# Optimization experiments

Hardware: AMD Instinct MI355X
Metric: run time of the kernel (lower is better)

## Reference

```python
import jax, jax.numpy as jnp
import numpy as np

NUM_HEADS = 12
DIM_HEAD = 64
SCALE = DIM_HEAD ** -0.5
LOG2PI = float(np.log(2.0 * np.pi))


def setup_inputs() -> dict:
    key = jax.random.key(0)
    k1, k2, k3, k4 = jax.random.split(key, 4)
    b, n, e = 2, 2048, 768
    inner = NUM_HEADS * DIM_HEAD
    return {
        "x": jax.random.normal(k1, (b, n, e), dtype=jnp.float32),
        "w_qkv": jax.random.normal(k2, (e, 3 * inner), dtype=jnp.float32) * (e ** -0.5),
        "w_out": jax.random.normal(k3, (inner, e), dtype=jnp.float32) * (inner ** -0.5),
        "b_out": jax.random.normal(k4, (e,), dtype=jnp.float32) * 0.02,
    }


def reference(x, w_qkv, w_out, b_out):
    b, n, _ = x.shape
    h, d = NUM_HEADS, DIM_HEAD
    qkv = x @ w_qkv  # (b, n, 3*h*d)
    q, k, v = jnp.split(qkv, 3, axis=-1)
    # (b, n, h*d) -> (b, h, n, d)
    to_heads = lambda t: t.reshape(b, n, h, d).transpose(0, 2, 1, 3)
    q, k, v = to_heads(q), to_heads(k), to_heads(v)

    dots = jnp.einsum("bhid,bhjd->bhij", q, k) * SCALE  # (b, h, n, n)
    attn = jax.nn.softmax(dots, axis=-1)
    product = jnp.einsum("bhij,bhjd->bhid", attn, v)  # (b, h, n, d)

    # cross-head statistics (torch.var is unbiased -> ddof=1)
    mean = jnp.mean(product, axis=1, keepdims=True)           # (b, 1, n, d)
    variance = jnp.var(product, axis=1, ddof=1, keepdims=True)  # (b, 1, n, d)

    log_probs = -0.5 * (LOG2PI + jnp.log(variance)
                        - 0.5 * (product - mean) ** 2 / variance)
    log_probs = jnp.sum(log_probs, axis=-1) \
        - jnp.sum(jnp.log(jnp.sqrt(variance)), axis=-1)  # (b, h, n)

    # second attn-weighted matmul, weighted by per-(b,h,n) log-likelihood
    out = jnp.einsum("bhij,bhjd->bhid", log_probs[..., None] * attn, v)
    out = out.transpose(0, 2, 1, 3).reshape(b, n, h * d)  # (b, n, h*d)
    return out @ w_out + b_out
```

## Files before the change

### kernel.cpp

```cpp
#include <hip/hip_runtime.h>

#define BB    2
#define NCTX  2048
#define EDIM  768
#define HH    12
#define DH    64
#define NQKV  2304
#define QSZ   (BB*HH*NCTX*DH)
#define GK    768
#define SCALE 0.125f
#define LOG2PI 1.8378770664093453f

typedef __bf16 bf16x8 __attribute__((ext_vector_type(8)));
typedef __bf16 bf16x4 __attribute__((ext_vector_type(4)));
typedef float  f32x4  __attribute__((ext_vector_type(4)));
typedef float  f32x16 __attribute__((ext_vector_type(16)));

#define GLOAD_LDS16(g, l)                                      \
  __builtin_amdgcn_global_load_lds(                            \
      (const __attribute__((address_space(1))) void*)(g),      \
      (__attribute__((address_space(3))) void*)(l), 16, 0, 0)

__device__ __forceinline__
void cvt_T_tile(const float* __restrict__ W, __bf16* __restrict__ WT,
                int R, int C, int c0, int r0, int t) {
  __shared__ float ts[32][33];
  const int rr = t >> 5, cc = t & 31;
  #pragma unroll
  for (int i = 0; i < 4; ++i)
    ts[rr + i*8][cc] = W[(size_t)(r0 + rr + i*8)*C + c0 + cc];
  __syncthreads();
  #pragma unroll
  for (int i = 0; i < 4; ++i)
    WT[(size_t)(c0 + rr + i*8)*R + r0 + cc] = (__bf16)ts[cc][rr + i*8];
}

__global__ __launch_bounds__(256)
void prep_all(const float* __restrict__ x, __bf16* __restrict__ xbf,
              const float* __restrict__ wqkv, const float* __restrict__ wout,
              __bf16* __restrict__ wqkvT, __bf16* __restrict__ woutT) {
  int b = blockIdx.x;
  if (b < 1536) {
    int i = b*256 + threadIdx.x;
    float4 a = *(const float4*)(x + (size_t)i*8);
    float4 c = *(const float4*)(x + (size_t)i*8 + 4);
    bf16x8 o;
    o[0]=(__bf16)a.x; o[1]=(__bf16)a.y; o[2]=(__bf16)a.z; o[3]=(__bf16)a.w;
    o[4]=(__bf16)c.x; o[5]=(__bf16)c.y; o[6]=(__bf16)c.z; o[7]=(__bf16)c.w;
    *(bf16x8*)(xbf + (size_t)i*8) = o;
  } else if (b < 3264) {
    b -= 1536;
    cvt_T_tile(wqkv, wqkvT, GK, NQKV, (b % 72)*32, (b / 72)*32, threadIdx.x);
  } else {
    b -= 3264;
    cvt_T_tile(wout, woutT, GK, EDIM, (b % 24)*32, (b / 24)*32, threadIdx.x);
  }
}

#define GSTAGE(t_, b_) do {                                                  \
    _Pragma("unroll")                                                        \
    for (int i_ = 0; i_ < 2; ++i_) {                                         \
      GLOAD_LDS16(Asrc + (size_t)i_*16*GK + (size_t)(t_)*32,                 \
                  dstA + (b_)*16384 + i_*1024);                              \
      GLOAD_LDS16(Bsrc + (size_t)i_*16*GK + (size_t)(t_)*32,                 \
                  dstB + (b_)*16384 + i_*1024);                              \
    } } while (0)

#define GITER(ki_, c_) do {                                                  \
    if ((ki_) < GK/32 - 1)                                                   \
      asm volatile("s_waitcnt vmcnt(4)" ::: "memory");                       \
    else                                                                     \
      asm volatile("s_waitcnt vmcnt(0)" ::: "memory");                       \
    __builtin_amdgcn_s_barrier();                                            \
    asm volatile("" ::: "memory");                                           \
    if ((ki_) + 2 < GK/32) GSTAGE((ki_) + 2, ((c_) + 2) % 3);                \
    const char* Asc = smem + (c_)*16384;                                     \
    const char* Bsc = Asc + 8192;                                            \
    bf16x8 af[4], bf[4];                                                     \
    _Pragma("unroll")                                                        \
    for (int mf = 0; mf < 4; ++mf) {                                         \
      int m = wr*64 + mf*16 + l15;                                           \
      af[mf] = *(const bf16x8*)(Asc + m*64 + ((g*16) ^ (((m>>1)&3)<<4)));    \
    }                                                                        \
    _Pragma("unroll")                                                        \
    for (int nf = 0; nf < 4; ++nf) {                                         \
      int n = wc*64 + nf*16 + l15;                                           \
      bf[nf] = *(const bf16x8*)(Bsc + n*64 + ((g*16) ^ (((n>>1)&3)<<4)));    \
    }                                                                        \
    __builtin_amdgcn_s_setprio(1);                                           \
    _Pragma("unroll")                                                        \
    for (int mf = 0; mf < 4; ++mf)                                           \
      _Pragma("unroll")                                                      \
      for (int nf = 0; nf < 4; ++nf)                                         \
        acc[mf][nf] = __builtin_amdgcn_mfma_f32_16x16x32_bf16(               \
            af[mf], bf[nf], acc[mf][nf], 0, 0, 0);                           \
    __builtin_amdgcn_s_setprio(0);                                           \
  } while (0)

#define GEMM_CORE(Aa, Bb, acc)                                               \
  const int lane = tid & 63, w = tid >> 6;                                   \
  const int l15 = lane & 15, g = lane >> 4;                                  \
  const int wr = w >> 1, wc = w & 1;                                         \
  const int lrow16 = lane >> 2;                                              \
  const int lsl = (lane & 3) ^ ((lane >> 3) & 3);                            \
  f32x4 acc[4][4];                                                           \
  _Pragma("unroll")                                                          \
  for (int i = 0; i < 4; ++i)                                                \
    _Pragma("unroll")                                                        \
    for (int j = 0; j < 4; ++j) acc[i][j] = (f32x4){0.f,0.f,0.f,0.f};        \
  const __bf16* Asrc = (Aa) + (size_t)(w*32 + lrow16)*GK + lsl*8;            \
  const __bf16* Bsrc = (Bb) + (size_t)(w*32 + lrow16)*GK + lsl*8;            \
  char* dstA = smem + w*2048;                                                \
  char* dstB = smem + 8192 + w*2048;                                         \
  GSTAGE(0, 0);                                                              \
  GSTAGE(1, 1);                                                              \
  for (int kb = 0; kb < GK/96; ++kb) {                 \
    GITER(kb*3 + 0, 0);                                                      \
    GITER(kb*3 + 1, 1);                                                      \
    GITER(kb*3 + 2, 2);                                                      \
  }

__global__ __launch_bounds__(256)
void gemm_qkv_mfma(const __bf16* __restrict__ A, const __bf16* __restrict__ BT,
                   __bf16* __restrict__ qb, __bf16* __restrict__ kb,
                   __bf16* __restrict__ vtb) {
  __shared__ __align__(16) char smem[3*16384];
  const int tid = threadIdx.x;
  const int xcd = blockIdx.x & 7, local = blockIdx.x >> 3;
  const int mb = (xcd & 3)*8 + local/9;
  const int nb = (xcd >> 2)*9 + local%9;
  const int m0 = mb*128, n0 = nb*128;
  GEMM_CORE(A + (size_t)m0*GK, BT + (size_t)n0*GK, acc)
  #pragma unroll
  for (int mf = 0; mf < 4; ++mf) {
    const int m0r = m0 + wr*64 + mf*16 + g*4;
    const int b_  = m0r >> 11, ii0 = m0r & 2047;
    #pragma unroll
    for (int nf = 0; nf < 4; ++nf) {
      const int c = n0 + wc*64 + nf*16 + l15;
      const int t = c / 768;
      const int rem = c - t*768;
      const int head = rem >> 6, dd = rem & 63;
      if (t == 0) {
        #pragma unroll
        for (int r = 0; r < 4; ++r)
          qb[((size_t)(b_*HH + head)*NCTX + ii0 + r)*DH + dd] =
              (__bf16)(acc[mf][nf][r] * SCALE);
      } else if (t == 1) {
        #pragma unroll
        for (int r = 0; r < 4; ++r)
          kb[((size_t)(b_*HH + head)*NCTX + ii0 + r)*DH + dd] =
              (__bf16)acc[mf][nf][r];
      } else {
        bf16x4 pv;
        pv[0] = (__bf16)acc[mf][nf][0];
        pv[1] = (__bf16)acc[mf][nf][1];
        pv[2] = (__bf16)acc[mf][nf][2];
        pv[3] = (__bf16)acc[mf][nf][3];
        *(bf16x4*)(vtb + ((size_t)(b_*HH + head)*DH + dd)*NCTX + ii0) = pv;
      }
    }
  }
}

__global__ __launch_bounds__(512)
void attn_mfma(const __bf16* __restrict__ Q, const __bf16* __restrict__ K,
               const __bf16* __restrict__ Vg, float* __restrict__ P) {
  __shared__ __align__(16) char smem[2*32768];
  const int id  = blockIdx.x;
  const int xcd = id & 7;
  const int jj  = id >> 3;
  const int bh  = xcd*3 + (jj >> 4);
  const int q0  = (jj & 15) * 128;
  const int tid = threadIdx.x;
  const int w = tid >> 6, lane = tid & 63;
  const int wq = w & 3, wk = w >> 2;
  const int l31 = lane & 31, hi = lane >> 5;
  const __bf16* Qb = Q  + (size_t)bh * NCTX * DH;
  const __bf16* Kb = K  + (size_t)bh * NCTX * DH;
  const __bf16* Vb = Vg + (size_t)bh * DH * NCTX;

  bf16x8 qa[4];
  {
    const __bf16* qr = Qb + (size_t)(q0 + wq*32 + l31)*DH + hi*8;
    #pragma unroll
    for (int s = 0; s < 4; ++s) qa[s] = *(const bf16x8*)(qr + s*16);
  }
  bf16x8 ones;
  #pragma unroll
  for (int j = 0; j < 8; ++j) ones[j] = (__bf16)1.0f;

  f32x16 oacc[2], lacc, zero16;
  #pragma unroll
  for (int i = 0; i < 16; ++i)
    { oacc[0][i] = 0.f; oacc[1][i] = 0.f; lacc[i] = 0.f; zero16[i] = 0.f; }

  const int lrow  = lane >> 3;
  const int lslot = (lane & 7) ^ lrow;
  const bool isK = (w < 4);
  const int wg = isK ? w : (w - 4);
  const __bf16* src0 = isK ? (Kb + (size_t)(wg*16 + lrow)*DH   + lslot*8)
                           : (Vb + (size_t)(wg*16 + lrow)*NCTX + lslot*8);
  const int dstoff = (isK ? 0 : 8192) + wg*2048;

  #define STAGE(kk_, s_) do {                                                 \
    char* sb = smem + (s_)*32768 + dstoff;                                    \
    if (isK) {                                                                \
      GLOAD_LDS16(src0 + (size_t)(kk_)*DH,          sb);                      \
      GLOAD_LDS16(src0 + (size_t)(kk_)*DH + 512,    sb + 1024);               \
      GLOAD_LDS16(src0 + (size_t)(kk_)*DH + 4096,   sb + 16384);              \
      GLOAD_LDS16(src0 + (size_t)(kk_)*DH + 4608,   sb + 16384 + 1024);       \
    } else {                                                                  \
      GLOAD_LDS16(src0 + (kk_),                     sb);                      \
      GLOAD_LDS16(src0 + (kk_) + 8*NCTX,            sb + 1024);               \
      GLOAD_LDS16(src0 + (kk_) + 64,                sb + 16384);              \
      GLOAD_LDS16(src0 + (kk_) + 64 + 8*NCTX,       sb + 16384 + 1024);       \
    }                                                                         \
  } while (0)

  #define CVTPK(dst, a, b) \
    asm("v_cvt_pk_bf16_f32 %0, %1, %2" : "=v"(dst) : "v"(a), "v"(b))

  #define ATTN_TILE(TB) do {                                                  \
    const char* Kl = (TB);                                                    \
    const char* Vt = (TB) + 8192;                                             \
    f32x16 sacc;                                                              \
    __builtin_amdgcn_s_setprio(1);                                            \
    {                                                                         \
      const int key = wk*32 + l31;                                            \
      const char* kbase = Kl + key*128;                                       \
      const int swz = (key&7) << 4;                                           \
      bf16x8 kf = *(const bf16x8*)(kbase + ((hi*16) ^ swz));                  \
      sacc = __builtin_amdgcn_mfma_f32_32x32x16_bf16(kf, qa[0], zero16, 0, 0, 0); \
      _Pragma("unroll")                                                       \
      for (int s = 1; s < 4; ++s) {                                           \
        kf = *(const bf16x8*)(kbase + ((s*32 + hi*16) ^ swz));                \
        sacc = __builtin_amdgcn_mfma_f32_32x32x16_bf16(kf, qa[s], sacc, 0, 0, 0); \
      }                                                                       \
    }                                                                         \
    __builtin_amdgcn_s_setprio(0);                                            \
    unsigned px0, px1, px2, px3, px4, px5, px6, px7;                          \
    {                                                                         \
      float e[16];                                                            \
      _Pragma("unroll")                                                       \
      for (int r = 0; r < 16; ++r) e[r] = __expf(sacc[r]);                    \
      CVTPK(px0, e[0],  e[1]);  CVTPK(px1, e[2],  e[3]);                      \
      CVTPK(px2, e[4],  e[5]);  CVTPK(px3, e[6],  e[7]);                      \
      CVTPK(px4, e[8],  e[9]);  CVTPK(px5, e[10], e[11]);                     \
      CVTPK(px6, e[12], e[13]); CVTPK(px7, e[14], e[15]);                     \
      asm("v_permlane32_swap_b32 %0, %1" : "+v"(px0), "+v"(px2));             \
      asm("v_permlane32_swap_b32 %0, %1" : "+v"(px1), "+v"(px3));             \
      asm("v_permlane32_swap_b32 %0, %1" : "+v"(px4), "+v"(px6));             \
      asm("v_permlane32_swap_b32 %0, %1" : "+v"(px5), "+v"(px7));             \
    }                                                                         \
    union PF { unsigned u[4]; bf16x8 v; };                                    \
    PF pf0, pf1;                                                              \
    pf0.u[0]=px0; pf0.u[1]=px1; pf0.u[2]=px2; pf0.u[3]=px3;                   \
    pf1.u[0]=px4; pf1.u[1]=px5; pf1.u[2]=px6; pf1.u[3]=px7;                   \
    __builtin_amdgcn_s_setprio(1);                                            \
    _Pragma("unroll")                                                         \
    for (int s = 0; s < 2; ++s) {                                             \
      bf16x8 pf = s ? pf1.v : pf0.v;                                          \
      lacc = __builtin_amdgcn_mfma_f32_32x32x16_bf16(pf, ones, lacc, 0, 0, 0);\
      _Pragma("unroll")                                                       \
      for (int nf = 0; nf < 2; ++nf) {                                        \
        int d = nf*32 + l31;                                                  \
        bf16x8 vf = *(const bf16x8*)(Vt + d*128 +                             \
            (((wk*32 + s*16 + hi*8)*2) ^ ((d&7)<<4)));                        \
        oacc[nf] = __builtin_amdgcn_mfma_f32_32x32x16_bf16(pf, vf, oacc[nf], 0, 0, 0); \
      }                                                                       \
    }                                                                         \
    __builtin_amdgcn_s_setprio(0);                                            \
  } while (0)

  STAGE(0, 0);

  for (int ts = 0; ts < NCTX/128; ++ts) {
    const int s = ts & 1;
    __syncthreads();
    if (ts + 1 < NCTX/128) STAGE((ts+1)*128, 1-s);
    const char* sb = smem + s*32768;
    ATTN_TILE(sb);
    ATTN_TILE(sb + 16384);
  }
  #undef STAGE
  #undef ATTN_TILE
  #undef CVTPK

  __syncthreads();
  float* scrO = (float*)smem;
  float* scrL = (float*)(smem + 32768);
  if (wk == 1) {
    #pragma unroll
    for (int nf = 0; nf < 2; ++nf)
      #pragma unroll
      for (int r = 0; r < 16; ++r)
        scrO[((wq*2 + nf)*16 + r)*64 + lane] = oacc[nf][r];
    #pragma unroll
    for (int r = 0; r < 16; ++r)
      scrL[(wq*16 + r)*64 + lane] = lacc[r];
  }
  __syncthreads();
  if (wk == 0) {
    #pragma unroll
    for (int r = 0; r < 16; ++r) {
      float linv = 1.0f / (lacc[r] + scrL[(wq*16 + r)*64 + lane]);
      int q = q0 + wq*32 + (r&3) + 8*(r>>2) + 4*hi;
      #pragma unroll
      for (int nf = 0; nf < 2; ++nf) {
        float o = oacc[nf][r] + scrO[((wq*2 + nf)*16 + r)*64 + lane];
        P[((size_t)bh*NCTX + q)*DH + nf*32 + l31] = o * linv;
      }
    }
  }
}

__global__ __launch_bounds__(256)
void stats_scale(const float* __restrict__ P, __bf16* __restrict__ Pbf) {
  const int bi = blockIdx.x*4 + (threadIdx.x >> 6);
  const int b_ = bi >> 11, i = bi & 2047;
  const int d = threadIdx.x & 63;
  const size_t hstride = (size_t)NCTX * DH;
  const size_t base = ((size_t)(b_*HH) * NCTX + i) * DH + d;
  float x[HH];
  #pragma unroll
  for (int h = 0; h < HH; ++h) x[h] = P[base + h*hstride];
  float sum = 0.f;
  #pragma unroll
  for (int h = 0; h < HH; ++h) sum += x[h];
  float mean = sum * (1.0f/12.0f);
  float ss = 0.f;
  #pragma unroll
  for (int h = 0; h < HH; ++h) { float t = x[h]-mean; ss += t*t; }
  float var = ss * (1.0f/11.0f);
  float lv = logf(var);
  float inv = 0.25f / var;
  __bf16* orow = Pbf + (size_t)bi * GK + d;
  #pragma unroll
  for (int h = 0; h < HH; ++h) {
    float t = x[h] - mean;
    float part = -0.5f*LOG2PI - lv + t*t*inv;
    #pragma unroll
    for (int off = 32; off; off >>= 1) part += __shfl_xor(part, off);
    orow[h*DH] = (__bf16)(part * x[h]);
  }
}

__global__ __launch_bounds__(256)
void gemm_out_mfma(const __bf16* __restrict__ A, const __bf16* __restrict__ BT,
                   const float* __restrict__ bias, float* __restrict__ out) {
  __shared__ __align__(16) char smem[3*16384];
  const int tid = threadIdx.x;
  const int xcd = blockIdx.x & 7, local = blockIdx.x >> 3;
  const int mb = (xcd & 3)*8 + local/3;
  const int nb = (xcd >> 2)*3 + local%3;
  const int m0 = mb*128, n0 = nb*128;
  GEMM_CORE(A + (size_t)m0*GK, BT + (size_t)n0*GK, acc)
  #pragma unroll
  for (int mf = 0; mf < 4; ++mf)
    #pragma unroll
    for (int nf = 0; nf < 4; ++nf)
      #pragma unroll
      for (int r = 0; r < 4; ++r) {
        int m = m0 + wr*64 + mf*16 + g*4 + r;
        int c = n0 + wc*64 + nf*16 + l15;
        out[(size_t)m*EDIM + c] = acc[mf][nf][r] + bias[c];
      }
}

extern "C" void kernel_launch(void* const* d_in, const int* in_sizes, int n_in,
                              void* d_out, int out_size, void* d_ws, size_t ws_size,
                              hipStream_t stream) {
  const float* x     = (const float*)d_in[0];
  const float* w_qkv = (const float*)d_in[1];
  const float* w_out = (const float*)d_in[2];
  const float* b_out = (const float*)d_in[3];
  float* out = (float*)d_out;

  __bf16* xbf   = (__bf16*)d_ws;
  __bf16* wqkvT = xbf   + (size_t)BB*NCTX*GK;
  __bf16* woutT = wqkvT + (size_t)NQKV*GK;
  __bf16* qb    = woutT + (size_t)EDIM*GK;
  __bf16* kb    = qb  + (size_t)QSZ;
  __bf16* vtb   = kb  + (size_t)QSZ;
  __bf16* Pbf   = vtb + (size_t)QSZ;
  float*  Pf    = (float*)(Pbf + (size_t)QSZ);

  prep_all<<<dim3(3840), 256, 0, stream>>>(x, xbf, w_qkv, w_out, wqkvT, woutT);
  gemm_qkv_mfma<<<dim3(576), 256, 0, stream>>>(xbf, wqkvT, qb, kb, vtb);
  attn_mfma<<<dim3(384), 512, 0, stream>>>(qb, kb, vtb, Pf);
  stats_scale<<<dim3(BB*NCTX/4), 256, 0, stream>>>(Pf, Pbf);
  gemm_out_mfma<<<dim3(192), 256, 0, stream>>>(Pbf, woutT, b_out, out);
}
```

Measured before the change: 95.67 us.

## Triple-buffer K/V tiles in attention with prefetch depth two and vmcnt waits

Replaces the double-buffered 128-key staging with a three-slot ring of 64-key tiles, prefetching two tiles ahead. Each iteration waits only for the oldest outstanding loads via s_waitcnt vmcnt(2) plus a raw barrier, instead of a full __syncthreads. The goal is to hide global-to-LDS latency better and shrink shared memory so occupancy may rise. In exchange it issues more barriers per key, and correctness now depends on the vmcnt accounting matching the loads in flight.

```diff
diff --git a/kernel.cpp b/kernel.cpp
--- a/kernel.cpp
+++ b/kernel.cpp
@@ -166,7 +166,7 @@
 __global__ __launch_bounds__(512)
 void attn_mfma(const __bf16* __restrict__ Q, const __bf16* __restrict__ K,
                const __bf16* __restrict__ Vg, float* __restrict__ P) {
-  __shared__ __align__(16) char smem[2*32768];
+  __shared__ __align__(16) char smem[3*16384];
   const int id  = blockIdx.x;
   const int xcd = id & 7;
   const int jj  = id >> 3;
@@ -203,18 +203,14 @@
                            : (Vb + (size_t)(wg*16 + lrow)*NCTX + lslot*8);
   const int dstoff = (isK ? 0 : 8192) + wg*2048;
 
-  #define STAGE(kk_, s_) do {                                                 \
-    char* sb = smem + (s_)*32768 + dstoff;                                    \
+  #define STAGE(kk_, b_) do {                                                 \
+    char* sb = smem + (b_)*16384 + dstoff;                                    \
     if (isK) {                                                                \
       GLOAD_LDS16(src0 + (size_t)(kk_)*DH,          sb);                      \
       GLOAD_LDS16(src0 + (size_t)(kk_)*DH + 512,    sb + 1024);               \
-      GLOAD_LDS16(src0 + (size_t)(kk_)*DH + 4096,   sb + 16384);              \
-      GLOAD_LDS16(src0 + (size_t)(kk_)*DH + 4608,   sb + 16384 + 1024);       \
     } else {                                                                  \
       GLOAD_LDS16(src0 + (kk_),                     sb);                      \
       GLOAD_LDS16(src0 + (kk_) + 8*NCTX,            sb + 1024);               \
-      GLOAD_LDS16(src0 + (kk_) + 64,                sb + 16384);              \
-      GLOAD_LDS16(src0 + (kk_) + 64 + 8*NCTX,       sb + 16384 + 1024);       \
     }                                                                         \
   } while (0)
 
@@ -273,18 +269,27 @@
     __builtin_amdgcn_s_setprio(0);                                            \
   } while (0)
 
+  #define AITER(t_, c_) do {                                                  \
+    if ((t_) < 31) asm volatile("s_waitcnt vmcnt(2)" ::: "memory");           \
+    else           asm volatile("s_waitcnt vmcnt(0)" ::: "memory");           \
+    __builtin_amdgcn_s_barrier();                                             \
+    asm volatile("" ::: "memory");                                            \
+    if ((t_) + 2 < 32) STAGE(((t_)+2)*64, ((c_)+2)%3);                        \
+    ATTN_TILE(smem + (c_)*16384);                                             \
+  } while (0)
+
   STAGE(0, 0);
-
-  for (int ts = 0; ts < NCTX/128; ++ts) {
-    const int s = ts & 1;
-    __syncthreads();
-    if (ts + 1 < NCTX/128) STAGE((ts+1)*128, 1-s);
-    const char* sb = smem + s*32768;
-    ATTN_TILE(sb);
-    ATTN_TILE(sb + 16384);
-  }
+  STAGE(64, 1);
+  for (int tb = 0; tb < 30; tb += 3) {
+    AITER(tb+0, 0);
+    AITER(tb+1, 1);
+    AITER(tb+2, 2);
+  }
+  AITER(30, 0);
+  AITER(31, 1);
+  #undef AITER
+  #undef ATTN_TILE
   #undef STAGE
-  #undef ATTN_TILE
   #undef CVTPK
 
   __syncthreads();
```

After: 95.68 us, median of 2. No clear change (+0.0%).
